# Optimization experiments

Hardware: AMD Instinct MI355X
Metric: run time of the kernel (lower is better)

The kernel has to match this reference:

```python
import jax, jax.numpy as jnp
import numpy as np
import math

H_HEAD = 8
D_MODEL = 1024
DEPTH = 12
D_K = D_MODEL // H_HEAD // 2  # 64
LAMBDA_INIT = 0.8 - 0.6 * math.exp(-0.3 * DEPTH)
EPS = 1e-5


def setup_inputs() -> dict:
    key = jax.random.key(0)
    ks = jax.random.split(key, 16)
    B, S, D = 2, 2048, D_MODEL
    std = 1.0 / math.sqrt(D)
    inp = {
        "query": jax.random.normal(ks[0], (B, S, D), jnp.float32),
        "key":   jax.random.normal(ks[1], (B, S, D), jnp.float32),
        "value": jax.random.normal(ks[2], (B, S, D), jnp.float32),
        "wq_w": jax.random.normal(ks[3], (D, D), jnp.float32) * std,
        "wq_b": jnp.zeros((D,), jnp.float32),
        "wk_w": jax.random.normal(ks[4], (D, D), jnp.float32) * std,
        "wk_b": jnp.zeros((D,), jnp.float32),
        "wv_w": jax.random.normal(ks[5], (D, D), jnp.float32) * std,
        "wv_b": jnp.zeros((D,), jnp.float32),
        "fc_w": jax.random.normal(ks[6], (D, D), jnp.float32) * std,
        "fc_b": jnp.zeros((D,), jnp.float32),
        "lambda_q1": jax.random.normal(ks[7], (D_K,), jnp.float32) * 0.1,
        "lambda_k1": jax.random.normal(ks[8], (D_K,), jnp.float32) * 0.1,
        "lambda_q2": jax.random.normal(ks[9], (D_K,), jnp.float32) * 0.1,
        "lambda_k2": jax.random.normal(ks[10], (D_K,), jnp.float32) * 0.1,
        "subln_w": jnp.ones((2 * D_K,), jnp.float32),
    }
    return inp


def _rms_norm(x, w):
    xf = x.astype(jnp.float32)
    out = xf * jax.lax.rsqrt(jnp.mean(xf * xf, axis=-1, keepdims=True) + EPS)
    return out.astype(x.dtype) * w


def reference(query, key, value, wq_w, wq_b, wk_w, wk_b, wv_w, wv_b,
              fc_w, fc_b, lambda_q1, lambda_k1, lambda_q2, lambda_k2, subln_w):
    B, S, D = query.shape
    h, dk = H_HEAD, D_K
    # projections (torch Linear: x @ W^T + b)
    q = (query @ wq_w.T + wq_b).reshape(B, S, 2 * h, dk).transpose(0, 2, 1, 3)   # [B,2h,S,dk]
    k = (key   @ wk_w.T + wk_b).reshape(B, S, 2 * h, dk).transpose(0, 2, 1, 3)   # [B,2h,S,dk]
    v = (value @ wv_w.T + wv_b).reshape(B, S, h, 2 * dk).transpose(0, 2, 1, 3)   # [B,h,S,2dk]

    scores = jnp.einsum('bhqd,bhkd->bhqk', q, k) / math.sqrt(dk)                 # [B,2h,S,S]
    aw = jax.nn.softmax(scores.astype(jnp.float32), axis=-1).astype(scores.dtype)

    lam1 = jnp.exp(jnp.sum(lambda_q1 * lambda_k1).astype(jnp.float32)).astype(q.dtype)
    lam2 = jnp.exp(jnp.sum(lambda_q2 * lambda_k2).astype(jnp.float32)).astype(q.dtype)
    lam = lam1 - lam2 + LAMBDA_INIT

    aw = aw.reshape(B, h, 2, S, S)
    aw = aw[:, :, 0] - lam * aw[:, :, 1]                                          # [B,h,S,S]

    attn = jnp.einsum('bhqk,bhkd->bhqd', aw, v)                                   # [B,h,S,2dk]
    attn = _rms_norm(attn, subln_w) * (1.0 - LAMBDA_INIT)
    attn = attn.transpose(0, 2, 1, 3).reshape(B, S, h * 2 * dk)
    out = attn @ fc_w.T + fc_b
    return (out, aw)
```

## Files before the change

kernel.cpp:

```cpp
#include <hip/hip_runtime.h>
#include <stdint.h>

#define DEV __device__ __forceinline__

typedef short s8v __attribute__((ext_vector_type(8)));
typedef float f4v __attribute__((ext_vector_type(4)));
typedef unsigned short u16;

static constexpr float LAMBDA_INIT = 0.783605766531624464f;
static constexpr float OUT_SCALE   = 0.216394233468375536f;

DEV u16 f2bf(float f) {
    uint32_t u = __builtin_bit_cast(uint32_t, f);
    u += 0x7fffu + ((u >> 16) & 1u);
    return (u16)(u >> 16);
}
DEV float bf2f(u16 v) {
    return __builtin_bit_cast(float, (uint32_t)v << 16);
}

__global__ __launch_bounds__(256)
void cvt_kernel(const float* __restrict__ q, const float* __restrict__ k,
                const float* __restrict__ v, const float* __restrict__ w0,
                const float* __restrict__ w1, const float* __restrict__ w2,
                const float* __restrict__ w3,
                u16* qo, u16* ko, u16* vo, u16* o0, u16* o1, u16* o2, u16* o3)
{
    int bid = blockIdx.x;
    const float* src; u16* dst; int base;
    if      (bid < 2048) { src = q;  dst = qo; base = bid * 2048; }
    else if (bid < 4096) { src = k;  dst = ko; base = (bid - 2048) * 2048; }
    else if (bid < 6144) { src = v;  dst = vo; base = (bid - 4096) * 2048; }
    else if (bid < 6656) { src = w0; dst = o0; base = (bid - 6144) * 2048; }
    else if (bid < 7168) { src = w1; dst = o1; base = (bid - 6656) * 2048; }
    else if (bid < 7680) { src = w2; dst = o2; base = (bid - 7168) * 2048; }
    else                 { src = w3; dst = o3; base = (bid - 7680) * 2048; }
    int i = base + threadIdx.x * 8;
    float4 a = *(const float4*)(src + i);
    float4 b = *(const float4*)(src + i + 4);
    u16 r[8] = { f2bf(a.x), f2bf(a.y), f2bf(a.z), f2bf(a.w),
                 f2bf(b.x), f2bf(b.y), f2bf(b.z), f2bf(b.w) };
    *(s8v*)(dst + i) = *(const s8v*)r;
}

template<int OUT_MODE>
__global__ __launch_bounds__(256)
void gemm128(const u16* __restrict__ A, const u16* __restrict__ W,
             const float* __restrict__ bias, void* __restrict__ Cp)
{
    constexpr int K = 1024;
    __shared__ __align__(16) char smem[OUT_MODE == 2 ? 32768 : 24576];
    const int m0 = blockIdx.x * 128, n0 = blockIdx.y * 64;
    const int t = threadIdx.x, lane = t & 63, wave = t >> 6;
    const int l15 = lane & 15, g = lane >> 4;

    f4v acc[2][4] = {};

    for (int k0 = 0; k0 < K; k0 += 64) {
#pragma unroll
        for (int i = 0; i < 4; ++i) {
            int idx = t + i * 256, row = idx >> 3, piece = idx & 7;
            s8v v = *(const s8v*)(A + (size_t)(m0 + row) * K + k0 + piece * 8);
            *(s8v*)(smem + row * 128 + ((piece * 16) ^ ((row & 7) << 4))) = v;
        }
#pragma unroll
        for (int i = 0; i < 2; ++i) {
            int idx = t + i * 256, row = idx >> 3, piece = idx & 7;
            s8v v = *(const s8v*)(W + (size_t)(n0 + row) * K + k0 + piece * 8);
            *(s8v*)(smem + 16384 + row * 128 + ((piece * 16) ^ ((row & 7) << 4))) = v;
        }
        __syncthreads();
#pragma unroll
        for (int ks = 0; ks < 2; ++ks) {
            s8v af[2], bf4[4];
#pragma unroll
            for (int mt = 0; mt < 2; ++mt) {
                int row = wave * 32 + mt * 16 + l15;
                af[mt] = *(const s8v*)(smem + row * 128 + ((ks * 64 + g * 16) ^ ((l15 & 7) << 4)));
            }
#pragma unroll
            for (int nt = 0; nt < 4; ++nt) {
                int row = nt * 16 + l15;
                bf4[nt] = *(const s8v*)(smem + 16384 + row * 128 + ((ks * 64 + g * 16) ^ ((l15 & 7) << 4)));
            }
#pragma unroll
            for (int mt = 0; mt < 2; ++mt)
#pragma unroll
                for (int nt = 0; nt < 4; ++nt)
                    acc[mt][nt] = __builtin_amdgcn_mfma_f32_16x16x32_bf16(af[mt], bf4[nt], acc[mt][nt], 0, 0, 0);
        }
        __syncthreads();
    }

    float bv[4];
#pragma unroll
    for (int nt = 0; nt < 4; ++nt) bv[nt] = bias[n0 + nt * 16 + l15];

    if (OUT_MODE == 0) {
        u16* rep = (u16*)smem;
#pragma unroll
        for (int mt = 0; mt < 2; ++mt)
#pragma unroll
            for (int nt = 0; nt < 4; ++nt)
#pragma unroll
                for (int r = 0; r < 4; ++r)
                    rep[(wave * 32 + mt * 16 + g * 4 + r) * 64 + nt * 16 + l15] = f2bf(acc[mt][nt][r] + bv[nt]);
        __syncthreads();
        u16* C = (u16*)Cp;
#pragma unroll
        for (int j = 0; j < 4; ++j) {
            int m = j * 32 + (t >> 3), chunk = t & 7;
            s8v v = *(const s8v*)(smem + m * 128 + chunk * 16);
            *(s8v*)(C + (size_t)(m0 + m) * 1024 + n0 + chunk * 8) = v;
        }
    } else if (OUT_MODE == 1) {
        u16* LT = (u16*)smem;
#pragma unroll
        for (int mt = 0; mt < 2; ++mt)
#pragma unroll
            for (int nt = 0; nt < 4; ++nt)
#pragma unroll
                for (int r = 0; r < 4; ++r)
                    LT[(nt * 16 + l15) * 136 + wave * 32 + mt * 16 + g * 4 + r] = f2bf(acc[mt][nt][r] + bv[nt]);
        __syncthreads();
        u16* C = (u16*)Cp;
        const int b = m0 >> 11, s0 = m0 & 2047;
#pragma unroll
        for (int j = 0; j < 4; ++j) {
            int n = j * 16 + (t >> 4), chunk = t & 15;
            s8v v = *(const s8v*)(smem + n * 272 + chunk * 16);
            *(s8v*)(C + ((size_t)b * 1024 + n0 + n) * 2048 + s0 + chunk * 8) = v;
        }
    } else {
        float* rep = (float*)smem;
#pragma unroll
        for (int mt = 0; mt < 2; ++mt)
#pragma unroll
            for (int nt = 0; nt < 4; ++nt)
#pragma unroll
                for (int r = 0; r < 4; ++r)
                    rep[(wave * 32 + mt * 16 + g * 4 + r) * 64 + nt * 16 + l15] = acc[mt][nt][r] + bv[nt];
        __syncthreads();
        float* C = (float*)Cp;
#pragma unroll
        for (int j = 0; j < 8; ++j) {
            int m = j * 16 + (t >> 4), c4 = t & 15;
            float4 v = *(const float4*)(smem + m * 256 + c4 * 16);
            *(float4*)(C + (size_t)(m0 + m) * 1024 + n0 + c4 * 4) = v;
        }
    }
}

__global__ __launch_bounds__(512, 4)
void attn_kernel(const u16* __restrict__ Qb, const u16* __restrict__ Kb,
                 const u16* __restrict__ Vt,
                 const float* __restrict__ lq1, const float* __restrict__ lk1,
                 const float* __restrict__ lq2, const float* __restrict__ lk2,
                 const float* __restrict__ subw, float* __restrict__ aw,
                 u16* __restrict__ an)
{
    constexpr int S = 2048, D = 1024;
    __shared__ __align__(16) char smem[75776];
    const int bid0 = blockIdx.x;
    const int bid = (bid0 & 7) * 64 + (bid0 >> 3);
    const int qt = bid & 31, h = (bid >> 5) & 7, b = bid >> 8;
    const int t = threadIdx.x, lane = t & 63, w = t >> 6;
    const int qw = w >> 1, kw = w & 1;
    const int l15 = lane & 15, g = lane >> 4;
    const int qrow0 = qt * 64, wrow0 = qrow0 + qw * 16;

    short* P   = (short*)(smem + 65536);
    float* sst = (float*)(smem + 74752);
    float* Po  = (float*)smem;

    float lam;
    {
        float p1 = lq1[lane] * lk1[lane], p2 = lq2[lane] * lk2[lane];
#pragma unroll
        for (int off = 1; off < 64; off <<= 1) {
            p1 += __shfl_xor(p1, off);
            p2 += __shfl_xor(p2, off);
        }
        lam = expf(p1) - expf(p2) + LAMBDA_INIT;
    }

    const u16* Qbase = Qb + ((size_t)b * S + wrow0 + l15) * D + h * 128;
    s8v q1[2], q2[2];
#pragma unroll
    for (int ks = 0; ks < 2; ++ks) {
        q1[ks] = *(const s8v*)(Qbase + ks * 32 + g * 8);
        q2[ks] = *(const s8v*)(Qbase + 64 + ks * 32 + g * 8);
    }
    const u16* Ksrc = Kb + (size_t)b * S * D + h * 128;
    const u16* Vsrc = Vt + ((size_t)b * 1024 + h * 128) * 2048;
    const int swz = (l15 & 7) << 4;

    float t1a[4] = {}, t2a[4] = {};
    s8v kreg[2], vreg[2];
#pragma unroll
    for (int i = 0; i < 2; ++i) {
        int idx = t + i * 512, row = idx >> 4, piece = idx & 15;
        kreg[i] = *(const s8v*)(Ksrc + (size_t)row * D + piece * 8);
    }
#pragma unroll
    for (int i = 0; i < 2; ++i) {
        int idx = t + i * 512, row = idx >> 4, piece = idx & 15;
        int sub = piece >> 3, colB = (piece & 7) * 16;
        *(s8v*)(smem + sub * 8192 + row * 128 + (colB ^ ((row & 7) << 4))) = kreg[i];
    }
#pragma unroll
    for (int i = 0; i < 2; ++i) {
        int idx = t + i * 512, row = idx >> 4, piece = idx & 15;
        kreg[i] = *(const s8v*)(Ksrc + (size_t)(64 + row) * D + piece * 8);
    }
    __syncthreads();

    for (int kt = 0; kt < 32; ++kt) {
        char* kcur = smem + (kt & 1) * 32768;
        char* knxt = smem + ((kt + 1) & 1) * 32768;
        if (kt < 31) {
#pragma unroll
            for (int i = 0; i < 2; ++i) {
                int idx = t + i * 512, row = idx >> 4, piece = idx & 15;
                int sub = piece >> 3, colB = (piece & 7) * 16;
                *(s8v*)(knxt + sub * 8192 + row * 128 + (colB ^ ((row & 7) << 4))) = kreg[i];
            }
        }
        if (kt < 30) {
            const u16* src = Ksrc + (size_t)(kt + 2) * 64 * D;
#pragma unroll
            for (int i = 0; i < 2; ++i) {
                int idx = t + i * 512, row = idx >> 4, piece = idx & 15;
                kreg[i] = *(const s8v*)(src + (size_t)row * D + piece * 8);
            }
        }
        f4v s1[2] = {}, s2[2] = {};
        __builtin_amdgcn_s_setprio(1);
#pragma unroll
        for (int nt = 0; nt < 2; ++nt)
#pragma unroll
            for (int ks = 0; ks < 2; ++ks) {
                int ro = (kw * 32 + nt * 16 + l15) * 128 + ((ks * 64 + g * 16) ^ swz);
                s1[nt] = __builtin_amdgcn_mfma_f32_16x16x32_bf16(q1[ks], *(const s8v*)(kcur + ro), s1[nt], 0, 0, 0);
                s2[nt] = __builtin_amdgcn_mfma_f32_16x16x32_bf16(q2[ks], *(const s8v*)(kcur + 8192 + ro), s2[nt], 0, 0, 0);
            }
        __builtin_amdgcn_s_setprio(0);
#pragma unroll
        for (int nt = 0; nt < 2; ++nt)
#pragma unroll
            for (int r = 0; r < 4; ++r) {
                t1a[r] += __expf(s1[nt][r] * 0.125f);
                t2a[r] += __expf(s2[nt][r] * 0.125f);
            }
        __syncthreads();
    }

#pragma unroll
    for (int r = 0; r < 4; ++r) {
#pragma unroll
        for (int off = 1; off < 16; off <<= 1) {
            t1a[r] += __shfl_xor(t1a[r], off);
            t2a[r] += __shfl_xor(t2a[r], off);
        }
    }
#pragma unroll
    for (int i = 0; i < 2; ++i) {
        int idx = t + i * 512;
        { int row = idx >> 4, piece = idx & 15;
          kreg[i] = *(const s8v*)(Ksrc + (size_t)row * D + piece * 8); }
        { int dd = idx >> 3, piece = idx & 7;
          vreg[i] = *(const s8v*)(Vsrc + (size_t)dd * 2048 + piece * 8); }
    }
    if (l15 == 0) {
#pragma unroll
        for (int r = 0; r < 4; ++r) {
            int row = g * 4 + r;
            sst[(w * 2 + 0) * 16 + row] = t1a[r];
            sst[(w * 2 + 1) * 16 + row] = t2a[r];
        }
    }
#pragma unroll
    for (int i = 0; i < 2; ++i) {
        int idx = t + i * 512;
        { int row = idx >> 4, piece = idx & 15;
          int sub = piece >> 3, colB = (piece & 7) * 16;
          *(s8v*)(smem + sub * 8192 + row * 128 + (colB ^ ((row & 7) << 4))) = kreg[i]; }
        { int dd = idx >> 3, piece = idx & 7;
          *(s8v*)(smem + 16384 + dd * 128 + ((piece * 16) ^ ((dd & 7) << 4))) = vreg[i]; }
    }
#pragma unroll
    for (int i = 0; i < 2; ++i) {
        int idx = t + i * 512;
        { int row = idx >> 4, piece = idx & 15;
          kreg[i] = *(const s8v*)(Ksrc + (size_t)(64 + row) * D + piece * 8); }
        { int dd = idx >> 3, piece = idx & 7;
          vreg[i] = *(const s8v*)(Vsrc + (size_t)dd * 2048 + 64 + piece * 8); }
    }
    __syncthreads();
    float il1[4], il2[4];
    {
        const int p = w ^ 1;
#pragma unroll
        for (int r = 0; r < 4; ++r) {
            int row = g * 4 + r;
            il1[r] = 1.f / (t1a[r] + sst[(p * 2 + 0) * 16 + row]);
            il2[r] = 1.f / (t2a[r] + sst[(p * 2 + 1) * 16 + row]);
        }
    }

    f4v po[8] = {};
    float* awb = aw + ((size_t)(b * 8 + h) * S + qrow0) * S;
    const int arow = lane >> 2, acol = kw * 32 + (lane & 3) * 8;

    for (int kt = 0; kt < 32; ++kt) {
        const int kv0 = kt * 64;
        char* cur = smem + (kt & 1) * 32768;
        char* nxt = smem + ((kt + 1) & 1) * 32768;
        if (kt < 31) {
#pragma unroll
            for (int i = 0; i < 2; ++i) {
                int idx = t + i * 512;
                { int row = idx >> 4, piece = idx & 15;
                  int sub = piece >> 3, colB = (piece & 7) * 16;
                  *(s8v*)(nxt + sub * 8192 + row * 128 + (colB ^ ((row & 7) << 4))) = kreg[i]; }
                { int dd = idx >> 3, piece = idx & 7;
                  *(s8v*)(nxt + 16384 + dd * 128 + ((piece * 16) ^ ((dd & 7) << 4))) = vreg[i]; }
            }
        }
        if (kt < 30) {
            const u16* ksp = Ksrc + (size_t)(kv0 + 128) * D;
            const u16* vsp = Vsrc + kv0 + 128;
#pragma unroll
            for (int i = 0; i < 2; ++i) {
                int idx = t + i * 512;
                { int row = idx >> 4, piece = idx & 15;
                  kreg[i] = *(const s8v*)(ksp + (size_t)row * D + piece * 8); }
                { int dd = idx >> 3, piece = idx & 7;
                  vreg[i] = *(const s8v*)(vsp + (size_t)dd * 2048 + piece * 8); }
            }
        }

        f4v s1[2] = {}, s2[2] = {};
        __builtin_amdgcn_s_setprio(1);
#pragma unroll
        for (int nt = 0; nt < 2; ++nt)
#pragma unroll
            for (int ks = 0; ks < 2; ++ks) {
                int ro = (kw * 32 + nt * 16 + l15) * 128 + ((ks * 64 + g * 16) ^ swz);
                s1[nt] = __builtin_amdgcn_mfma_f32_16x16x32_bf16(q1[ks], *(const s8v*)(cur + ro), s1[nt], 0, 0, 0);
                s2[nt] = __builtin_amdgcn_mfma_f32_16x16x32_bf16(q2[ks], *(const s8v*)(cur + 8192 + ro), s2[nt], 0, 0, 0);
            }
        __builtin_amdgcn_s_setprio(0);
#pragma unroll
        for (int nt = 0; nt < 2; ++nt)
#pragma unroll
            for (int r = 0; r < 4; ++r) {
                float p1 = __expf(s1[nt][r] * 0.125f) * il1[r];
                float p2 = __expf(s2[nt][r] * 0.125f) * il2[r];
                P[(qw * 16 + g * 4 + r) * 72 + kw * 32 + nt * 16 + l15] = (short)f2bf(p1 - lam * p2);
            }
        s8v pf = *(const s8v*)(P + (qw * 16 + l15) * 72 + kw * 32 + g * 8);
        __builtin_amdgcn_s_setprio(1);
#pragma unroll
        for (int dn = 0; dn < 8; ++dn) {
            const s8v* vf = (const s8v*)(cur + 16384 + (dn * 16 + l15) * 128 + ((kw * 64 + g * 16) ^ swz));
            po[dn] = __builtin_amdgcn_mfma_f32_16x16x32_bf16(pf, *vf, po[dn], 0, 0, 0);
        }
        __builtin_amdgcn_s_setprio(0);
        {
            s8v a = *(const s8v*)(P + (qw * 16 + arow) * 72 + acol);
            float4 o0 = { bf2f((u16)a[0]), bf2f((u16)a[1]), bf2f((u16)a[2]), bf2f((u16)a[3]) };
            float4 o1 = { bf2f((u16)a[4]), bf2f((u16)a[5]), bf2f((u16)a[6]), bf2f((u16)a[7]) };
            float* dp = awb + (size_t)(qw * 16 + arow) * S + kv0 + acol;
            *(float4*)dp = o0;
            *(float4*)(dp + 4) = o1;
        }
        __syncthreads();
    }

    if (kw == 0) {
#pragma unroll
        for (int dn = 0; dn < 8; ++dn)
#pragma unroll
            for (int r = 0; r < 4; ++r)
                Po[(qw * 16 + g * 4 + r) * 128 + dn * 16 + l15] = po[dn][r];
    }
    __syncthreads();
    if (kw == 1) {
#pragma unroll
        for (int dn = 0; dn < 8; ++dn)
#pragma unroll
            for (int r = 0; r < 4; ++r)
                Po[(qw * 16 + g * 4 + r) * 128 + dn * 16 + l15] += po[dn][r];
    }
    __syncthreads();

    {
        const int row = t >> 3, c0 = (t & 7) * 16;
        float ss = 0.f;
#pragma unroll
        for (int j = 0; j < 4; ++j) {
            float4 v4 = *(const float4*)(Po + row * 128 + c0 + j * 4);
            ss += v4.x * v4.x + v4.y * v4.y + v4.z * v4.z + v4.w * v4.w;
        }
#pragma unroll
        for (int off = 1; off < 8; off <<= 1) ss += __shfl_xor(ss, off);
        float rs = rsqrtf(ss * (1.0f / 128.0f) + 1e-5f) * OUT_SCALE;
        u16* dst = an + ((size_t)b * S + qrow0 + row) * D + h * 128;
#pragma unroll
        for (int j = 0; j < 2; ++j) {
            u16 tmp[8];
#pragma unroll
            for (int e = 0; e < 8; ++e) {
                int c = c0 + j * 8 + e;
                tmp[e] = f2bf(Po[row * 128 + c] * rs * subw[c]);
            }
            *(s8v*)(dst + c0 + j * 8) = *(const s8v*)tmp;
        }
    }
}

extern "C" void kernel_launch(void* const* d_in, const int* in_sizes, int n_in,
                              void* d_out, int out_size, void* d_ws, size_t ws_size,
                              hipStream_t stream)
{
    const float* query = (const float*)d_in[0];
    const float* key   = (const float*)d_in[1];
    const float* value = (const float*)d_in[2];
    const float* wq_w  = (const float*)d_in[3];
    const float* wq_b  = (const float*)d_in[4];
    const float* wk_w  = (const float*)d_in[5];
    const float* wk_b  = (const float*)d_in[6];
    const float* wv_w  = (const float*)d_in[7];
    const float* wv_b  = (const float*)d_in[8];
    const float* fc_w  = (const float*)d_in[9];
    const float* fc_b  = (const float*)d_in[10];
    const float* lq1   = (const float*)d_in[11];
    const float* lk1   = (const float*)d_in[12];
    const float* lq2   = (const float*)d_in[13];
    const float* lk2   = (const float*)d_in[14];
    const float* subw  = (const float*)d_in[15];

    const size_t MB = 1024 * 1024;
    char* ws = (char*)d_ws;
    u16*   Qbf = (u16*)(ws);
    u16*   Kbf = (u16*)(ws + 8 * MB);
    u16*   Vtg = (u16*)(ws + 16 * MB);
    u16*   ANb = (u16*)(ws + 24 * MB);
    u16*   wqb = (u16*)(ws + 32 * MB);
    u16*   wkb = (u16*)(ws + 34 * MB);
    u16*   wvb = (u16*)(ws + 36 * MB);
    u16*   fcb = (u16*)(ws + 38 * MB);

    float* out0 = (float*)d_out;
    float* awp  = out0 + (size_t)4096 * 1024;
    u16* qx = (u16*)awp;
    u16* kx = qx + (size_t)4096 * 1024;
    u16* vx = kx + (size_t)4096 * 1024;

    cvt_kernel<<<dim3(8192), dim3(256), 0, stream>>>(query, key, value, wq_w, wk_w, wv_w, fc_w,
                                                     qx, kx, vx, wqb, wkb, wvb, fcb);
    dim3 grid(32, 16), blk(256);
    gemm128<0><<<grid, blk, 0, stream>>>(qx, wqb, wq_b, Qbf);
    gemm128<0><<<grid, blk, 0, stream>>>(kx, wkb, wk_b, Kbf);
    gemm128<1><<<grid, blk, 0, stream>>>(vx, wvb, wv_b, Vtg);
    attn_kernel<<<dim3(512), dim3(512), 0, stream>>>(Qbf, Kbf, Vtg, lq1, lk1, lq2, lk2,
                                                     subw, awp, ANb);
    gemm128<2><<<grid, blk, 0, stream>>>(ANb, fcb, fc_b, out0);
}
```

Baseline: 194.7 us.

## Split softmax-denominator pass into separate split-K kernel with partial sums

Moves the first attention pass, which sums exp(QK^T) for the softmax denominators, out of attn_kernel into a new attn_sum kernel. The new kernel splits the key range into four slices across 2048 blocks and writes per-slice partial sums to a workspace buffer that reuses the already-consumed wq bf16 region. attn_kernel then reads and adds the partials instead of running its own serial 32-tile pass. The aim is more parallelism for the reduction pass than 512 blocks looping over all keys gave. The cost is an extra launch, reloading Q, a small global round-trip for the partial sums, and reliance on that workspace region being free at that point.

```diff
diff --git a/kernel.cpp b/kernel.cpp
--- a/kernel.cpp
+++ b/kernel.cpp
@@ -151,16 +151,110 @@
     }
 }
 
+__global__ __launch_bounds__(256, 4)
+void attn_sum(const u16* __restrict__ Qb, const u16* __restrict__ Kb,
+              float* __restrict__ psum)
+{
+    constexpr int S = 2048, D = 1024;
+    __shared__ __align__(16) char smem[16384];
+    const int bid0 = blockIdx.x;
+    const int bid = (bid0 & 7) * 256 + (bid0 >> 3);
+    const int sl = bid & 3, qt = (bid >> 2) & 31, h = (bid >> 7) & 7, b = bid >> 10;
+    const int t = threadIdx.x, lane = t & 63, qw = t >> 6;
+    const int l15 = lane & 15, g = lane >> 4;
+    const int wrow0 = qt * 64 + qw * 16;
+
+    const u16* Qbase = Qb + ((size_t)b * S + wrow0 + l15) * D + h * 128;
+    s8v q1[2], q2[2];
+#pragma unroll
+    for (int ks = 0; ks < 2; ++ks) {
+        q1[ks] = *(const s8v*)(Qbase + ks * 32 + g * 8);
+        q2[ks] = *(const s8v*)(Qbase + 64 + ks * 32 + g * 8);
+    }
+    const u16* Ksrc = Kb + (size_t)b * S * D + (size_t)(sl * 512) * D + h * 128;
+    const int swz = (l15 & 7) << 4;
+
+    float t1a[4] = {}, t2a[4] = {};
+    s8v kreg[4];
+#pragma unroll
+    for (int i = 0; i < 4; ++i) {
+        int idx = t + i * 256, row = idx >> 4, piece = idx & 15;
+        kreg[i] = *(const s8v*)(Ksrc + (size_t)row * D + piece * 8);
+    }
+#pragma unroll
+    for (int i = 0; i < 4; ++i) {
+        int idx = t + i * 256, row = idx >> 4, piece = idx & 15;
+        int sub = piece >> 3, colB = (piece & 7) * 16;
+        *(s8v*)(smem + sub * 8192 + row * 128 + (colB ^ ((row & 7) << 4))) = kreg[i];
+    }
+
+    for (int kt = 0; kt < 8; ++kt) {
+        if (kt < 7) {
+            const u16* src = Ksrc + (size_t)(kt + 1) * 64 * D;
+#pragma unroll
+            for (int i = 0; i < 4; ++i) {
+                int idx = t + i * 256, row = idx >> 4, piece = idx & 15;
+                kreg[i] = *(const s8v*)(src + (size_t)row * D + piece * 8);
+            }
+        }
+        __syncthreads();
+        f4v s1[4] = {}, s2[4] = {};
+        __builtin_amdgcn_s_setprio(1);
+#pragma unroll
+        for (int nt = 0; nt < 4; ++nt)
+#pragma unroll
+            for (int ks = 0; ks < 2; ++ks) {
+                int ro = (nt * 16 + l15) * 128 + ((ks * 64 + g * 16) ^ swz);
+                s1[nt] = __builtin_amdgcn_mfma_f32_16x16x32_bf16(q1[ks], *(const s8v*)(smem + ro), s1[nt], 0, 0, 0);
+                s2[nt] = __builtin_amdgcn_mfma_f32_16x16x32_bf16(q2[ks], *(const s8v*)(smem + 8192 + ro), s2[nt], 0, 0, 0);
+            }
+        __builtin_amdgcn_s_setprio(0);
+#pragma unroll
+        for (int nt = 0; nt < 4; ++nt)
+#pragma unroll
+            for (int r = 0; r < 4; ++r) {
+                t1a[r] += __expf(s1[nt][r] * 0.125f);
+                t2a[r] += __expf(s2[nt][r] * 0.125f);
+            }
+        __syncthreads();
+        if (kt < 7) {
+#pragma unroll
+            for (int i = 0; i < 4; ++i) {
+                int idx = t + i * 256, row = idx >> 4, piece = idx & 15;
+                int sub = piece >> 3, colB = (piece & 7) * 16;
+                *(s8v*)(smem + sub * 8192 + row * 128 + (colB ^ ((row & 7) << 4))) = kreg[i];
+            }
+        }
+    }
+
+#pragma unroll
+    for (int r = 0; r < 4; ++r) {
+#pragma unroll
+        for (int off = 1; off < 16; off <<= 1) {
+            t1a[r] += __shfl_xor(t1a[r], off);
+            t2a[r] += __shfl_xor(t2a[r], off);
+        }
+    }
+    if (l15 == 0) {
+        float* pp = psum + (size_t)(((b * 8 + h) * 2048) + wrow0 + g * 4) * 8;
+#pragma unroll
+        for (int r = 0; r < 4; ++r) {
+            pp[r * 8 + sl]     = t1a[r];
+            pp[r * 8 + 4 + sl] = t2a[r];
+        }
+    }
+}
+
 __global__ __launch_bounds__(512, 4)
 void attn_kernel(const u16* __restrict__ Qb, const u16* __restrict__ Kb,
-                 const u16* __restrict__ Vt,
+                 const u16* __restrict__ Vt, const float* __restrict__ psum,
                  const float* __restrict__ lq1, const float* __restrict__ lk1,
                  const float* __restrict__ lq2, const float* __restrict__ lk2,
                  const float* __restrict__ subw, float* __restrict__ aw,
                  u16* __restrict__ an)
 {
     constexpr int S = 2048, D = 1024;
-    __shared__ __align__(16) char smem[75776];
+    __shared__ __align__(16) char smem[74752];
     const int bid0 = blockIdx.x;
     const int bid = (bid0 & 7) * 64 + (bid0 >> 3);
     const int qt = bid & 31, h = (bid >> 5) & 7, b = bid >> 8;
@@ -169,9 +263,8 @@
     const int l15 = lane & 15, g = lane >> 4;
     const int qrow0 = qt * 64, wrow0 = qrow0 + qw * 16;
 
-    short* P   = (short*)(smem + 65536);
-    float* sst = (float*)(smem + 74752);
-    float* Po  = (float*)smem;
+    short* P  = (short*)(smem + 65536);
+    float* Po = (float*)smem;
 
     float lam;
     {
@@ -195,74 +288,19 @@
     const u16* Vsrc = Vt + ((size_t)b * 1024 + h * 128) * 2048;
     const int swz = (l15 & 7) << 4;
 
-    float t1a[4] = {}, t2a[4] = {};
+    float il1[4], il2[4];
+    {
+        const float* pp = psum + (size_t)(((b * 8 + h) * 2048) + wrow0 + g * 4) * 8;
+#pragma unroll
+        for (int r = 0; r < 4; ++r) {
+            float4 a = *(const float4*)(pp + r * 8);
+            float4 c = *(const float4*)(pp + r * 8 + 4);
+            il1[r] = 1.f / ((a.x + a.y) + (a.z + a.w));
+            il2[r] = 1.f / ((c.x + c.y) + (c.z + c.w));
+        }
+    }
+
     s8v kreg[2], vreg[2];
-#pragma unroll
-    for (int i = 0; i < 2; ++i) {
-        int idx = t + i * 512, row = idx >> 4, piece = idx & 15;
-        kreg[i] = *(const s8v*)(Ksrc + (size_t)row * D + piece * 8);
-    }
-#pragma unroll
-    for (int i = 0; i < 2; ++i) {
-        int idx = t + i * 512, row = idx >> 4, piece = idx & 15;
-        int sub = piece >> 3, colB = (piece & 7) * 16;
-        *(s8v*)(smem + sub * 8192 + row * 128 + (colB ^ ((row & 7) << 4))) = kreg[i];
-    }
-#pragma unroll
-    for (int i = 0; i < 2; ++i) {
-        int idx = t + i * 512, row = idx >> 4, piece = idx & 15;
-        kreg[i] = *(const s8v*)(Ksrc + (size_t)(64 + row) * D + piece * 8);
-    }
-    __syncthreads();
-
-    for (int kt = 0; kt < 32; ++kt) {
-        char* kcur = smem + (kt & 1) * 32768;
-        char* knxt = smem + ((kt + 1) & 1) * 32768;
-        if (kt < 31) {
-#pragma unroll
-            for (int i = 0; i < 2; ++i) {
-                int idx = t + i * 512, row = idx >> 4, piece = idx & 15;
-                int sub = piece >> 3, colB = (piece & 7) * 16;
-                *(s8v*)(knxt + sub * 8192 + row * 128 + (colB ^ ((row & 7) << 4))) = kreg[i];
-            }
-        }
-        if (kt < 30) {
-            const u16* src = Ksrc + (size_t)(kt + 2) * 64 * D;
-#pragma unroll
-            for (int i = 0; i < 2; ++i) {
-                int idx = t + i * 512, row = idx >> 4, piece = idx & 15;
-                kreg[i] = *(const s8v*)(src + (size_t)row * D + piece * 8);
-            }
-        }
-        f4v s1[2] = {}, s2[2] = {};
-        __builtin_amdgcn_s_setprio(1);
-#pragma unroll
-        for (int nt = 0; nt < 2; ++nt)
-#pragma unroll
-            for (int ks = 0; ks < 2; ++ks) {
-                int ro = (kw * 32 + nt * 16 + l15) * 128 + ((ks * 64 + g * 16) ^ swz);
-                s1[nt] = __builtin_amdgcn_mfma_f32_16x16x32_bf16(q1[ks], *(const s8v*)(kcur + ro), s1[nt], 0, 0, 0);
-                s2[nt] = __builtin_amdgcn_mfma_f32_16x16x32_bf16(q2[ks], *(const s8v*)(kcur + 8192 + ro), s2[nt], 0, 0, 0);
-            }
-        __builtin_amdgcn_s_setprio(0);
-#pragma unroll
-        for (int nt = 0; nt < 2; ++nt)
-#pragma unroll
-            for (int r = 0; r < 4; ++r) {
-                t1a[r] += __expf(s1[nt][r] * 0.125f);
-                t2a[r] += __expf(s2[nt][r] * 0.125f);
-            }
-        __syncthreads();
-    }
-
-#pragma unroll
-    for (int r = 0; r < 4; ++r) {
-#pragma unroll
-        for (int off = 1; off < 16; off <<= 1) {
-            t1a[r] += __shfl_xor(t1a[r], off);
-            t2a[r] += __shfl_xor(t2a[r], off);
-        }
-    }
 #pragma unroll
     for (int i = 0; i < 2; ++i) {
         int idx = t + i * 512;
@@ -270,14 +308,6 @@
           kreg[i] = *(const s8v*)(Ksrc + (size_t)row * D + piece * 8); }
         { int dd = idx >> 3, piece = idx & 7;
           vreg[i] = *(const s8v*)(Vsrc + (size_t)dd * 2048 + piece * 8); }
-    }
-    if (l15 == 0) {
-#pragma unroll
-        for (int r = 0; r < 4; ++r) {
-            int row = g * 4 + r;
-            sst[(w * 2 + 0) * 16 + row] = t1a[r];
-            sst[(w * 2 + 1) * 16 + row] = t2a[r];
-        }
     }
 #pragma unroll
     for (int i = 0; i < 2; ++i) {
@@ -297,16 +327,6 @@
           vreg[i] = *(const s8v*)(Vsrc + (size_t)dd * 2048 + 64 + piece * 8); }
     }
     __syncthreads();
-    float il1[4], il2[4];
-    {
-        const int p = w ^ 1;
-#pragma unroll
-        for (int r = 0; r < 4; ++r) {
-            int row = g * 4 + r;
-            il1[r] = 1.f / (t1a[r] + sst[(p * 2 + 0) * 16 + row]);
-            il2[r] = 1.f / (t2a[r] + sst[(p * 2 + 1) * 16 + row]);
-        }
-    }
 
     f4v po[8] = {};
     float* awb = aw + ((size_t)(b * 8 + h) * S + qrow0) * S;
@@ -451,6 +471,7 @@
     u16*   wkb = (u16*)(ws + 34 * MB);
     u16*   wvb = (u16*)(ws + 36 * MB);
     u16*   fcb = (u16*)(ws + 38 * MB);
+    float* psum = (float*)(ws + 32 * MB);
 
     float* out0 = (float*)d_out;
     float* awp  = out0 + (size_t)4096 * 1024;
@@ -464,7 +485,8 @@
     gemm128<0><<<grid, blk, 0, stream>>>(qx, wqb, wq_b, Qbf);
     gemm128<0><<<grid, blk, 0, stream>>>(kx, wkb, wk_b, Kbf);
     gemm128<1><<<grid, blk, 0, stream>>>(vx, wvb, wv_b, Vtg);
-    attn_kernel<<<dim3(512), dim3(512), 0, stream>>>(Qbf, Kbf, Vtg, lq1, lk1, lq2, lk2,
+    attn_sum<<<dim3(2048), dim3(256), 0, stream>>>(Qbf, Kbf, psum);
+    attn_kernel<<<dim3(512), dim3(512), 0, stream>>>(Qbf, Kbf, Vtg, psum, lq1, lk1, lq2, lk2,
                                                      subw, awp, ANb);
     gemm128<2><<<grid, blk, 0, stream>>>(ANb, fcb, fc_b, out0);
 }
```

After: 196.1 us. No clear change (+0.7%).
